# Performance work log

Hardware: AMD Instinct MI355X
Metric: run time of the kernel (lower is better)

The kernel has to match this reference:

```python
import jax, jax.numpy as jnp
import numpy as np


def setup_inputs() -> dict:
    key = jax.random.key(0)
    ks = jax.random.split(key, 7)
    B, N, D, A = 32, 128, 512, 512
    sD = 1.0 / np.sqrt(D)
    sA = 1.0 / np.sqrt(A)
    return {
        "x": jax.random.normal(ks[0], (B, N, D), dtype=jnp.float32),
        "W1": jax.random.normal(ks[1], (A, D), dtype=jnp.float32) * sD,
        "b1": jax.random.normal(ks[2], (A,), dtype=jnp.float32) * sD,
        "W2": jax.random.normal(ks[3], (A, D), dtype=jnp.float32) * sD,
        "b2": jax.random.normal(ks[4], (A,), dtype=jnp.float32) * sD,
        "Wout": jax.random.normal(ks[5], (A,), dtype=jnp.float32) * sA,
        "bout": jax.random.normal(ks[6], (1,), dtype=jnp.float32) * sA,
    }


def reference(x, W1, b1, W2, b2, Wout, bout):
    # x: (B, N, D)
    x1 = jnp.einsum('bnd,ad->bna', x, W1) + b1  # mlp1 -> (B, N, A)
    x2 = jnp.einsum('bnd,ad->bna', x, W2) + b2  # mlp2 -> (B, N, A)
    # outer broadcast add: x1.unsqueeze(1) + x2.unsqueeze(2) -> (B, N, N, A)
    s = x1[:, None, :, :] + x2[:, :, None, :]
    # include_root=False: drop ROOT row along dim 1 -> (B, N-1, N, A)
    s = s[:, 1:, :, :]
    s = jnp.tanh(s)
    # out linear A -> 1, then squeeze -> (B, N-1, N)
    return jnp.einsum('bija,a->bij', s, Wout) + bout[0]
```

## Files before the change

kernel.cpp:

```cpp
#include <hip/hip_runtime.h>
#include <hip/hip_bf16.h>

#define B_ 32
#define N_ 128
#define D_ 512
#define A_ 512
#define R_ (B_*N_)
#define OC 1024
#define CEXP 2.8853900817779268f

typedef __attribute__((ext_vector_type(8))) short  frag_ab;
typedef __attribute__((ext_vector_type(4))) float  frag_cd;

__device__ inline unsigned pack2bf(float a, float b) {
    unsigned ua = __builtin_bit_cast(unsigned, a) + 0x8000u;
    unsigned ub = __builtin_bit_cast(unsigned, b) + 0x8000u;
    return __builtin_amdgcn_perm(ub, ua, 0x07060302);
}
__device__ inline float bf2f_lo(unsigned u){ return __builtin_bit_cast(float, u << 16); }
__device__ inline float bf2f_hi(unsigned u){ return __builtin_bit_cast(float, u & 0xffff0000u); }

__global__ __launch_bounds__(256) void k0_cvt(
    const float* __restrict__ X, const float* __restrict__ W1,
    const float* __restrict__ W2,
    unsigned short* __restrict__ Xb, unsigned short* __restrict__ W1b,
    unsigned short* __restrict__ W2b)
{
    const int NX = R_*D_/8, NW = A_*D_/8;
    int i = blockIdx.x*256 + threadIdx.x;
    const float* src; unsigned short* dst; int off;
    if (i < NX)            { src = X;  dst = Xb;  off = i; }
    else if (i < NX+NW)    { src = W1; dst = W1b; off = i-NX; }
    else if (i < NX+2*NW)  { src = W2; dst = W2b; off = i-NX-NW; }
    else return;
    float4 a = ((const float4*)src)[off*2];
    float4 c = ((const float4*)src)[off*2+1];
    uint4 o;
    o.x = pack2bf(a.x,a.y); o.y = pack2bf(a.z,a.w);
    o.z = pack2bf(c.x,c.y); o.w = pack2bf(c.z,c.w);
    ((uint4*)dst)[off] = o;
}

#define BK1 64
#define LDK 68

__global__ __launch_bounds__(256) void k1_mfma(
    const unsigned short* __restrict__ Xb,
    const unsigned short* __restrict__ W1b, const float* __restrict__ b1,
    const unsigned short* __restrict__ W2b, const float* __restrict__ b2,
    unsigned short* __restrict__ Yb)
{
    __shared__ unsigned short As[2][64*LDK];
    __shared__ unsigned short Bs[2][64*LDK];

    const int t = threadIdx.x, lane = t&63, wid = t>>6;
    const int wr = wid>>1, wc = wid&1;
    const int row0 = blockIdx.x*64, col0 = blockIdx.y*64;
    const unsigned short* Wb = (col0 < A_) ? W1b : W2b;
    const float* bb = (col0 < A_) ? b1 : b2;
    const int wrow0 = col0 & (A_-1);

    const int srow = t>>3;
    const int scol = (t&7)*8;

    frag_cd acc[2][2];
#pragma unroll
    for (int i=0;i<2;++i)
#pragma unroll
        for (int j=0;j<2;++j) acc[i][j] = frag_cd{0.f,0.f,0.f,0.f};

    const int fr = lane&15, g8 = (lane>>4)*8;

    uint4 ra[2], rb[2];
#pragma unroll
    for (int q=0;q<2;++q){
        int r = q*32 + srow;
        ra[q] = *(const uint4*)&Xb[(size_t)(row0 +r)*D_ + scol];
        rb[q] = *(const uint4*)&Wb[(size_t)(wrow0+r)*D_ + scol];
    }
#pragma unroll
    for (int q=0;q<2;++q){
        int r = q*32 + srow;
        *(uint4*)&As[0][r*LDK + scol] = ra[q];
        *(uint4*)&Bs[0][r*LDK + scol] = rb[q];
    }
    __syncthreads();

#pragma unroll
    for (int s=0; s<8; ++s) {
        const int cur = s&1;
        if (s<7) {
            const int k0 = (s+1)*BK1;
#pragma unroll
            for (int q=0;q<2;++q){
                int r = q*32 + srow;
                ra[q] = *(const uint4*)&Xb[(size_t)(row0 +r)*D_ + k0 + scol];
                rb[q] = *(const uint4*)&Wb[(size_t)(wrow0+r)*D_ + k0 + scol];
            }
        }
        frag_ab af[2][2], bf[2][2];
#pragma unroll
        for (int fi=0;fi<2;++fi)
#pragma unroll
            for (int ks=0;ks<2;++ks) {
                af[fi][ks] = *(const frag_ab*)&As[cur][(wr*32+fi*16+fr)*LDK + ks*32 + g8];
                bf[fi][ks] = *(const frag_ab*)&Bs[cur][(wc*32+fi*16+fr)*LDK + ks*32 + g8];
            }
#pragma unroll
        for (int ks=0;ks<2;++ks)
#pragma unroll
            for (int fi=0;fi<2;++fi)
#pragma unroll
                for (int fj=0;fj<2;++fj)
                    acc[fi][fj] = __builtin_amdgcn_mfma_f32_16x16x32_bf16(
                        af[fi][ks], bf[fj][ks], acc[fi][fj], 0, 0, 0);
        if (s<7) {
#pragma unroll
            for (int q=0;q<2;++q){
                int r = q*32 + srow;
                *(uint4*)&As[cur^1][r*LDK + scol] = ra[q];
                *(uint4*)&Bs[cur^1][r*LDK + scol] = rb[q];
            }
        }
        __syncthreads();
    }

#pragma unroll
    for (int fi=0;fi<2;++fi){
        const int rr = row0 + wr*32 + fi*16 + (lane>>4)*4;
#pragma unroll
        for (int fj=0;fj<2;++fj){
            const int cc = col0 + wc*32 + fj*16 + (lane&15);
            const float bias = bb[cc & (A_-1)];
#pragma unroll
            for (int r=0;r<4;++r){
                float e = __builtin_amdgcn_exp2f(CEXP*(acc[fi][fj][r] + bias));
                Yb[(size_t)(rr+r)*OC + cc] =
                    (unsigned short)((__builtin_bit_cast(unsigned, e) + 0x8000u) >> 16);
            }
        }
    }
}

#define ACH 128
#define LDA2 (ACH+4)

__global__ __launch_bounds__(256) void k2_tanh(
    const unsigned short* __restrict__ Yb,
    const float* __restrict__ Wout, const float* __restrict__ bout,
    float* __restrict__ out)
{
    __shared__ float e1s[32][LDA2];
    __shared__ float e2s[16][LDA2];
    __shared__ float wo[A_];
    __shared__ float wsum_s[4];

    const int t  = threadIdx.x;
    const int jt = blockIdx.x;
    const int it = blockIdx.y;
    const int b  = blockIdx.z;

    float wsacc = 0.f;
    for (int k=t; k<A_; k+=256){ float w = Wout[k]; wo[k] = w; wsacc += w; }
#pragma unroll
    for (int off=32; off>=1; off>>=1) wsacc += __shfl_down(wsacc, off, 64);
    if ((t&63)==0) wsum_s[t>>6] = wsacc;

    const unsigned short* yb = Yb + (size_t)b*N_*OC;
    const int sr = t>>4;
    const int sc = (t&15)*8;

    uint4 p1a = *(const uint4*)&yb[(size_t)(jt*32 + sr     )*OC + sc];
    uint4 p1b = *(const uint4*)&yb[(size_t)(jt*32 + sr + 16)*OC + sc];
    int i2c = it*16 + sr + 1; if (i2c > 127) i2c = 127;
    uint4 p2  = *(const uint4*)&yb[(size_t)i2c*OC + A_ + sc];
    {
        uint4 v = p1a;
        *(float4*)&e1s[sr][sc]   = float4{bf2f_lo(v.x),bf2f_hi(v.x),bf2f_lo(v.y),bf2f_hi(v.y)};
        *(float4*)&e1s[sr][sc+4] = float4{bf2f_lo(v.z),bf2f_hi(v.z),bf2f_lo(v.w),bf2f_hi(v.w)};
        v = p1b;
        *(float4*)&e1s[sr+16][sc]   = float4{bf2f_lo(v.x),bf2f_hi(v.x),bf2f_lo(v.y),bf2f_hi(v.y)};
        *(float4*)&e1s[sr+16][sc+4] = float4{bf2f_lo(v.z),bf2f_hi(v.z),bf2f_lo(v.w),bf2f_hi(v.w)};
        v = p2;
        *(float4*)&e2s[sr][sc]   = float4{bf2f_lo(v.x),bf2f_hi(v.x),bf2f_lo(v.y),bf2f_hi(v.y)};
        *(float4*)&e2s[sr][sc+4] = float4{bf2f_lo(v.z),bf2f_hi(v.z),bf2f_lo(v.w),bf2f_hi(v.w)};
    }
    __syncthreads();

    const int jl = t&15, il = t>>4;
    float a00 = 0.f, a01 = 0.f;

#pragma unroll
    for (int ch=0; ch<4; ++ch) {
        if (ch<3) {
            const int a0n = (ch+1)*ACH;
            p1a = *(const uint4*)&yb[(size_t)(jt*32 + sr     )*OC + a0n + sc];
            p1b = *(const uint4*)&yb[(size_t)(jt*32 + sr + 16)*OC + a0n + sc];
            p2  = *(const uint4*)&yb[(size_t)i2c*OC + A_ + a0n + sc];
        }
        const int a0 = ch*ACH;
#pragma unroll 4
        for (int c=0; c<ACH; c+=4) {
            float4 u0 = *(const float4*)&e1s[jl     ][c];
            float4 u1 = *(const float4*)&e1s[jl + 16][c];
            float4 v0 = *(const float4*)&e2s[il     ][c];
            float4 w  = *(const float4*)&wo[a0 + c];
            a00 += w.x * __builtin_amdgcn_rcpf(fmaf(u0.x, v0.x, 1.f));
            a01 += w.x * __builtin_amdgcn_rcpf(fmaf(u1.x, v0.x, 1.f));
            a00 += w.y * __builtin_amdgcn_rcpf(fmaf(u0.y, v0.y, 1.f));
            a01 += w.y * __builtin_amdgcn_rcpf(fmaf(u1.y, v0.y, 1.f));
            a00 += w.z * __builtin_amdgcn_rcpf(fmaf(u0.z, v0.z, 1.f));
            a01 += w.z * __builtin_amdgcn_rcpf(fmaf(u1.z, v0.z, 1.f));
            a00 += w.w * __builtin_amdgcn_rcpf(fmaf(u0.w, v0.w, 1.f));
            a01 += w.w * __builtin_amdgcn_rcpf(fmaf(u1.w, v0.w, 1.f));
        }
        if (ch<3) {
            __syncthreads();
            uint4 v = p1a;
            *(float4*)&e1s[sr][sc]   = float4{bf2f_lo(v.x),bf2f_hi(v.x),bf2f_lo(v.y),bf2f_hi(v.y)};
            *(float4*)&e1s[sr][sc+4] = float4{bf2f_lo(v.z),bf2f_hi(v.z),bf2f_lo(v.w),bf2f_hi(v.w)};
            v = p1b;
            *(float4*)&e1s[sr+16][sc]   = float4{bf2f_lo(v.x),bf2f_hi(v.x),bf2f_lo(v.y),bf2f_hi(v.y)};
            *(float4*)&e1s[sr+16][sc+4] = float4{bf2f_lo(v.z),bf2f_hi(v.z),bf2f_lo(v.w),bf2f_hi(v.w)};
            v = p2;
            *(float4*)&e2s[sr][sc]   = float4{bf2f_lo(v.x),bf2f_hi(v.x),bf2f_lo(v.y),bf2f_hi(v.y)};
            *(float4*)&e2s[sr][sc+4] = float4{bf2f_lo(v.z),bf2f_hi(v.z),bf2f_lo(v.w),bf2f_hi(v.w)};
            __syncthreads();
        }
    }

    const float wsum = wsum_s[0] + wsum_s[1] + wsum_s[2] + wsum_s[3];
    const float bo   = bout[0];
    const int i0 = it*16 + il;
    const int j0 = jt*32 + jl;

    if (i0 < 127) {
        out[((size_t)(b*127) + i0) * 128 + j0     ] = wsum - 2.f*a00 + bo;
        out[((size_t)(b*127) + i0) * 128 + j0 + 16] = wsum - 2.f*a01 + bo;
    }
}

extern "C" void kernel_launch(void* const* d_in, const int* in_sizes, int n_in,
                              void* d_out, int out_size, void* d_ws, size_t ws_size,
                              hipStream_t stream) {
    const float* x    = (const float*)d_in[0];
    const float* W1   = (const float*)d_in[1];
    const float* b1   = (const float*)d_in[2];
    const float* W2   = (const float*)d_in[3];
    const float* b2   = (const float*)d_in[4];
    const float* Wout = (const float*)d_in[5];
    const float* bout = (const float*)d_in[6];
    float* out = (float*)d_out;

    char* ws = (char*)d_ws;
    unsigned short* Yb  = (unsigned short*)ws;
    unsigned short* Xb  = (unsigned short*)(ws + (8u<<20));
    unsigned short* W1b = (unsigned short*)(ws + (12u<<20));
    unsigned short* W2b = (unsigned short*)(ws + (12u<<20) + (1u<<19));

    k0_cvt<<<1280, 256, 0, stream>>>(x, W1, W2, Xb, W1b, W2b);

    dim3 g1(R_/64, OC/64);
    k1_mfma<<<g1, 256, 0, stream>>>(Xb, W1b, b1, W2b, b2, Yb);

    dim3 g2(4, 8, B_);
    k2_tanh<<<g2, 256, 0, stream>>>(Yb, Wout, bout, out);
}
```

Before: 115.6 us.

## Enlarge k2 tile to 32x32 outputs per block with double-buffered LDS

Each thread in the tanh/reduction kernel now computes a 2x2 block of outputs instead of 2x1, so every e1/e2 value read from LDS feeds more reciprocal evaluations. The grid's i dimension is halved to match. The LDS staging is double-buffered, which drops one __syncthreads per chunk. The trade-off is fewer blocks (512 instead of 1024), which may reduce occupancy and latency hiding, plus more registers and LDS per block.

```diff
diff --git a/kernel.cpp b/kernel.cpp
--- a/kernel.cpp
+++ b/kernel.cpp
@@ -150,8 +150,8 @@
     const float* __restrict__ Wout, const float* __restrict__ bout,
     float* __restrict__ out)
 {
-    __shared__ float e1s[32][LDA2];
-    __shared__ float e2s[16][LDA2];
+    __shared__ float e1s[2][32][LDA2];
+    __shared__ float e2s[2][32][LDA2];
     __shared__ float wo[A_];
     __shared__ float wsum_s[4];
 
@@ -169,74 +169,98 @@
     const unsigned short* yb = Yb + (size_t)b*N_*OC;
     const int sr = t>>4;
     const int sc = (t&15)*8;
-
-    uint4 p1a = *(const uint4*)&yb[(size_t)(jt*32 + sr     )*OC + sc];
-    uint4 p1b = *(const uint4*)&yb[(size_t)(jt*32 + sr + 16)*OC + sc];
-    int i2c = it*16 + sr + 1; if (i2c > 127) i2c = 127;
-    uint4 p2  = *(const uint4*)&yb[(size_t)i2c*OC + A_ + sc];
+    int i2a = it*32 + sr + 1;      if (i2a > 127) i2a = 127;
+    int i2b = it*32 + sr + 17;     if (i2b > 127) i2b = 127;
+
     {
-        uint4 v = p1a;
-        *(float4*)&e1s[sr][sc]   = float4{bf2f_lo(v.x),bf2f_hi(v.x),bf2f_lo(v.y),bf2f_hi(v.y)};
-        *(float4*)&e1s[sr][sc+4] = float4{bf2f_lo(v.z),bf2f_hi(v.z),bf2f_lo(v.w),bf2f_hi(v.w)};
-        v = p1b;
-        *(float4*)&e1s[sr+16][sc]   = float4{bf2f_lo(v.x),bf2f_hi(v.x),bf2f_lo(v.y),bf2f_hi(v.y)};
-        *(float4*)&e1s[sr+16][sc+4] = float4{bf2f_lo(v.z),bf2f_hi(v.z),bf2f_lo(v.w),bf2f_hi(v.w)};
-        v = p2;
-        *(float4*)&e2s[sr][sc]   = float4{bf2f_lo(v.x),bf2f_hi(v.x),bf2f_lo(v.y),bf2f_hi(v.y)};
-        *(float4*)&e2s[sr][sc+4] = float4{bf2f_lo(v.z),bf2f_hi(v.z),bf2f_lo(v.w),bf2f_hi(v.w)};
+        uint4 v1a = *(const uint4*)&yb[(size_t)(jt*32 + sr     )*OC + sc];
+        uint4 v1b = *(const uint4*)&yb[(size_t)(jt*32 + sr + 16)*OC + sc];
+        uint4 v2a = *(const uint4*)&yb[(size_t)i2a*OC + A_ + sc];
+        uint4 v2b = *(const uint4*)&yb[(size_t)i2b*OC + A_ + sc];
+        uint4 v = v1a;
+        *(float4*)&e1s[0][sr][sc]   = float4{bf2f_lo(v.x),bf2f_hi(v.x),bf2f_lo(v.y),bf2f_hi(v.y)};
+        *(float4*)&e1s[0][sr][sc+4] = float4{bf2f_lo(v.z),bf2f_hi(v.z),bf2f_lo(v.w),bf2f_hi(v.w)};
+        v = v1b;
+        *(float4*)&e1s[0][sr+16][sc]   = float4{bf2f_lo(v.x),bf2f_hi(v.x),bf2f_lo(v.y),bf2f_hi(v.y)};
+        *(float4*)&e1s[0][sr+16][sc+4] = float4{bf2f_lo(v.z),bf2f_hi(v.z),bf2f_lo(v.w),bf2f_hi(v.w)};
+        v = v2a;
+        *(float4*)&e2s[0][sr][sc]   = float4{bf2f_lo(v.x),bf2f_hi(v.x),bf2f_lo(v.y),bf2f_hi(v.y)};
+        *(float4*)&e2s[0][sr][sc+4] = float4{bf2f_lo(v.z),bf2f_hi(v.z),bf2f_lo(v.w),bf2f_hi(v.w)};
+        v = v2b;
+        *(float4*)&e2s[0][sr+16][sc]   = float4{bf2f_lo(v.x),bf2f_hi(v.x),bf2f_lo(v.y),bf2f_hi(v.y)};
+        *(float4*)&e2s[0][sr+16][sc+4] = float4{bf2f_lo(v.z),bf2f_hi(v.z),bf2f_lo(v.w),bf2f_hi(v.w)};
     }
     __syncthreads();
 
     const int jl = t&15, il = t>>4;
-    float a00 = 0.f, a01 = 0.f;
+    float a00=0.f, a01=0.f, a10=0.f, a11=0.f;
 
 #pragma unroll
     for (int ch=0; ch<4; ++ch) {
+        const int cur = ch&1;
+        uint4 v1a, v1b, v2a, v2b;
         if (ch<3) {
             const int a0n = (ch+1)*ACH;
-            p1a = *(const uint4*)&yb[(size_t)(jt*32 + sr     )*OC + a0n + sc];
-            p1b = *(const uint4*)&yb[(size_t)(jt*32 + sr + 16)*OC + a0n + sc];
-            p2  = *(const uint4*)&yb[(size_t)i2c*OC + A_ + a0n + sc];
+            v1a = *(const uint4*)&yb[(size_t)(jt*32 + sr     )*OC + a0n + sc];
+            v1b = *(const uint4*)&yb[(size_t)(jt*32 + sr + 16)*OC + a0n + sc];
+            v2a = *(const uint4*)&yb[(size_t)i2a*OC + A_ + a0n + sc];
+            v2b = *(const uint4*)&yb[(size_t)i2b*OC + A_ + a0n + sc];
         }
         const int a0 = ch*ACH;
 #pragma unroll 4
         for (int c=0; c<ACH; c+=4) {
-            float4 u0 = *(const float4*)&e1s[jl     ][c];
-            float4 u1 = *(const float4*)&e1s[jl + 16][c];
-            float4 v0 = *(const float4*)&e2s[il     ][c];
+            float4 u0 = *(const float4*)&e1s[cur][jl     ][c];
+            float4 u1 = *(const float4*)&e1s[cur][jl + 16][c];
+            float4 v0 = *(const float4*)&e2s[cur][il     ][c];
+            float4 v1 = *(const float4*)&e2s[cur][il + 16][c];
             float4 w  = *(const float4*)&wo[a0 + c];
             a00 += w.x * __builtin_amdgcn_rcpf(fmaf(u0.x, v0.x, 1.f));
             a01 += w.x * __builtin_amdgcn_rcpf(fmaf(u1.x, v0.x, 1.f));
+            a10 += w.x * __builtin_amdgcn_rcpf(fmaf(u0.x, v1.x, 1.f));
+            a11 += w.x * __builtin_amdgcn_rcpf(fmaf(u1.x, v1.x, 1.f));
             a00 += w.y * __builtin_amdgcn_rcpf(fmaf(u0.y, v0.y, 1.f));
             a01 += w.y * __builtin_amdgcn_rcpf(fmaf(u1.y, v0.y, 1.f));
+            a10 += w.y * __builtin_amdgcn_rcpf(fmaf(u0.y, v1.y, 1.f));
+            a11 += w.y * __builtin_amdgcn_rcpf(fmaf(u1.y, v1.y, 1.f));
             a00 += w.z * __builtin_amdgcn_rcpf(fmaf(u0.z, v0.z, 1.f));
             a01 += w.z * __builtin_amdgcn_rcpf(fmaf(u1.z, v0.z, 1.f));
+            a10 += w.z * __builtin_amdgcn_rcpf(fmaf(u0.z, v1.z, 1.f));
+            a11 += w.z * __builtin_amdgcn_rcpf(fmaf(u1.z, v1.z, 1.f));
             a00 += w.w * __builtin_amdgcn_rcpf(fmaf(u0.w, v0.w, 1.f));
             a01 += w.w * __builtin_amdgcn_rcpf(fmaf(u1.w, v0.w, 1.f));
+            a10 += w.w * __builtin_amdgcn_rcpf(fmaf(u0.w, v1.w, 1.f));
+            a11 += w.w * __builtin_amdgcn_rcpf(fmaf(u1.w, v1.w, 1.f));
         }
         if (ch<3) {
-            __syncthreads();
-            uint4 v = p1a;
-            *(float4*)&e1s[sr][sc]   = float4{bf2f_lo(v.x),bf2f_hi(v.x),bf2f_lo(v.y),bf2f_hi(v.y)};
-            *(float4*)&e1s[sr][sc+4] = float4{bf2f_lo(v.z),bf2f_hi(v.z),bf2f_lo(v.w),bf2f_hi(v.w)};
-            v = p1b;
-            *(float4*)&e1s[sr+16][sc]   = float4{bf2f_lo(v.x),bf2f_hi(v.x),bf2f_lo(v.y),bf2f_hi(v.y)};
-            *(float4*)&e1s[sr+16][sc+4] = float4{bf2f_lo(v.z),bf2f_hi(v.z),bf2f_lo(v.w),bf2f_hi(v.w)};
-            v = p2;
-            *(float4*)&e2s[sr][sc]   = float4{bf2f_lo(v.x),bf2f_hi(v.x),bf2f_lo(v.y),bf2f_hi(v.y)};
-            *(float4*)&e2s[sr][sc+4] = float4{bf2f_lo(v.z),bf2f_hi(v.z),bf2f_lo(v.w),bf2f_hi(v.w)};
+            const int nxt = cur^1;
+            uint4 v = v1a;
+            *(float4*)&e1s[nxt][sr][sc]   = float4{bf2f_lo(v.x),bf2f_hi(v.x),bf2f_lo(v.y),bf2f_hi(v.y)};
+            *(float4*)&e1s[nxt][sr][sc+4] = float4{bf2f_lo(v.z),bf2f_hi(v.z),bf2f_lo(v.w),bf2f_hi(v.w)};
+            v = v1b;
+            *(float4*)&e1s[nxt][sr+16][sc]   = float4{bf2f_lo(v.x),bf2f_hi(v.x),bf2f_lo(v.y),bf2f_hi(v.y)};
+            *(float4*)&e1s[nxt][sr+16][sc+4] = float4{bf2f_lo(v.z),bf2f_hi(v.z),bf2f_lo(v.w),bf2f_hi(v.w)};
+            v = v2a;
+            *(float4*)&e2s[nxt][sr][sc]   = float4{bf2f_lo(v.x),bf2f_hi(v.x),bf2f_lo(v.y),bf2f_hi(v.y)};
+            *(float4*)&e2s[nxt][sr][sc+4] = float4{bf2f_lo(v.z),bf2f_hi(v.z),bf2f_lo(v.w),bf2f_hi(v.w)};
+            v = v2b;
+            *(float4*)&e2s[nxt][sr+16][sc]   = float4{bf2f_lo(v.x),bf2f_hi(v.x),bf2f_lo(v.y),bf2f_hi(v.y)};
+            *(float4*)&e2s[nxt][sr+16][sc+4] = float4{bf2f_lo(v.z),bf2f_hi(v.z),bf2f_lo(v.w),bf2f_hi(v.w)};
             __syncthreads();
         }
     }
 
     const float wsum = wsum_s[0] + wsum_s[1] + wsum_s[2] + wsum_s[3];
     const float bo   = bout[0];
-    const int i0 = it*16 + il;
+    const int i0 = it*32 + il;
     const int j0 = jt*32 + jl;
 
     if (i0 < 127) {
         out[((size_t)(b*127) + i0) * 128 + j0     ] = wsum - 2.f*a00 + bo;
         out[((size_t)(b*127) + i0) * 128 + j0 + 16] = wsum - 2.f*a01 + bo;
+    }
+    if (i0 + 16 < 127) {
+        out[((size_t)(b*127) + i0 + 16) * 128 + j0     ] = wsum - 2.f*a10 + bo;
+        out[((size_t)(b*127) + i0 + 16) * 128 + j0 + 16] = wsum - 2.f*a11 + bo;
     }
 }
 
@@ -263,6 +287,6 @@
     dim3 g1(R_/64, OC/64);
     k1_mfma<<<g1, 256, 0, stream>>>(Xb, W1b, b1, W2b, b2, Yb);
 
-    dim3 g2(4, 8, B_);
+    dim3 g2(4, 4, B_);
     k2_tanh<<<g2, 256, 0, stream>>>(Yb, Wout, bout, out);
 }
```

Result: no change. 117.7 us (+1.8%).
